# Kernel optimization log

Hardware: AMD Instinct MI355X
Metric: run time of the kernel (lower is better)

## Reference

```python
import jax, jax.numpy as jnp
import numpy as np

NUM_HEADS = 16
D_MODEL = 1024
HEAD_DIM = D_MODEL // NUM_HEADS
SCALE = float(np.sqrt(HEAD_DIM))  # NOTE: original multiplies q by sqrt(head_dim)
EPS = 1e-5


def layernorm(x, g, b):
    # LayerNorm over last dim (head_dim), learnable affine
    mu = jnp.mean(x, axis=-1, keepdims=True)
    var = jnp.mean(jnp.square(x - mu), axis=-1, keepdims=True)
    return (x - mu) * jax.lax.rsqrt(var + EPS) * g + b


def setup_inputs() -> dict:
    key = jax.random.key(0)
    ks = jax.random.split(key, 8)
    B, Nq, Nc = 2, 2048, 2048
    s = 0.02
    return {
        "x_query": jax.random.normal(ks[0], (B, Nq, D_MODEL), jnp.float32),
        "x_context": jax.random.normal(ks[1], (B, Nc, D_MODEL), jnp.float32),
        "Wq": jax.random.normal(ks[2], (D_MODEL, D_MODEL), jnp.float32) * s,
        "Wkv": jax.random.normal(ks[3], (D_MODEL, 2 * D_MODEL), jnp.float32) * s,
        "Wp": jax.random.normal(ks[4], (D_MODEL, D_MODEL), jnp.float32) * s,
        "bp": jnp.zeros((D_MODEL,), jnp.float32),
        "ln_g": jnp.ones((HEAD_DIM,), jnp.float32),
        "ln_b": jnp.zeros((HEAD_DIM,), jnp.float32),
    }


def reference(x_query, x_context, Wq, Wkv, Wp, bp, ln_g, ln_b):
    B, Nq, _ = x_query.shape
    Nc = x_context.shape[1]
    H, D = NUM_HEADS, HEAD_DIM
    # projections
    q = (x_query @ Wq).reshape(B, Nq, H, D).transpose(0, 2, 1, 3)  # b h n d
    kv = (x_context @ Wkv).reshape(B, Nc, 2, H, D)
    k = kv[:, :, 0].transpose(0, 2, 1, 3)  # b h n d
    v = kv[:, :, 1].transpose(0, 2, 1, 3)
    # QK-LayerNorm (shared params)
    q = layernorm(q, ln_g, ln_b)
    k = layernorm(k, ln_g, ln_b)
    # NOTE: faithful to source — q is MULTIPLIED by sqrt(head_dim)
    q = q * SCALE
    attn = jnp.einsum("bhqd,bhkd->bhqk", q, k)
    attn = jax.nn.softmax(attn, axis=-1)
    out = jnp.einsum("bhqk,bhkd->bhqd", attn, v)
    out = out.transpose(0, 2, 1, 3).reshape(B, Nq, H * D)
    return out @ Wp + bp
```

## Files before the change

kernel.cpp:

```cpp
#include <hip/hip_runtime.h>
#include <stdint.h>

#define NUM_HEADS 16
#define HEAD_DIM 64
#define D_MODEL 1024
#define SEQ 2048
#define BATCH 2

typedef unsigned short u16;
typedef __bf16 bf16x8 __attribute__((ext_vector_type(8)));
typedef _Float16 f16x8 __attribute__((ext_vector_type(8)));
typedef float f32x4 __attribute__((ext_vector_type(4)));

__device__ __forceinline__ u16 f2bf(float f) {
    union { float f; uint32_t u; } v; v.f = f;
    uint32_t u = v.u;
    u += 0x7FFFu + ((u >> 16) & 1u);
    return (u16)(u >> 16);
}
__device__ __forceinline__ float bf2f(u16 h) {
    union { uint32_t u; float f; } v; v.u = (uint32_t)h << 16; return v.f;
}
__device__ __forceinline__ u16 f2h(float f) {
    _Float16 h = (_Float16)f;
    return __builtin_bit_cast(u16, h);
}

__device__ __forceinline__ bf16x8 ld8(const u16* p) {
    return *reinterpret_cast<const bf16x8*>(p);
}
__device__ __forceinline__ f16x8 ld8h(const u16* p) {
    return *reinterpret_cast<const f16x8*>(p);
}

__device__ __forceinline__ void gl_lds16(const void* g, void* l) {
    __builtin_amdgcn_global_load_lds(
        (const __attribute__((address_space(1))) void*)g,
        (__attribute__((address_space(3))) void*)l,
        16, 0, 0);
}

template <int CTRL>
__device__ __forceinline__ float dpp_mov(float x) {
    return __builtin_bit_cast(float,
        __builtin_amdgcn_update_dpp(0, __builtin_bit_cast(int, x), CTRL, 0xf, 0xf, true));
}
__device__ __forceinline__ float rowsum16(float x) {
    x += dpp_mov<0x121>(x);
    x += dpp_mov<0x122>(x);
    x += dpp_mov<0x124>(x);
    x += dpp_mov<0x128>(x);
    return x;
}

__global__ __launch_bounds__(256) void k_cast_f16(const float* __restrict__ a,
                                                  const float* __restrict__ b,
                                                  u16* __restrict__ a16,
                                                  u16* __restrict__ b16, int n4each) {
    int i = blockIdx.x * 256 + threadIdx.x;
    const float* src; u16* dst; int j;
    if (i < n4each) { src = a; dst = a16; j = i; }
    else            { src = b; dst = b16; j = i - n4each; }
    float4 v = reinterpret_cast<const float4*>(src)[j];
    ushort4 o;
    o.x = f2h(v.x); o.y = f2h(v.y); o.z = f2h(v.z); o.w = f2h(v.w);
    reinterpret_cast<ushort4*>(dst)[j] = o;
}

__global__ __launch_bounds__(256) void k_transpose_bf16(const float* __restrict__ W,
                                                        u16* __restrict__ WT,
                                                        int K, int N) {
    __shared__ float tile[32][33];
    int bn = blockIdx.x * 32;
    int bk = blockIdx.y * 32;
    int tx = threadIdx.x & 31;
    int ty = threadIdx.x >> 5;
#pragma unroll
    for (int i = 0; i < 32; i += 8)
        tile[ty + i][tx] = W[(size_t)(bk + ty + i) * N + bn + tx];
    __syncthreads();
#pragma unroll
    for (int i = 0; i < 32; i += 8)
        WT[(size_t)(bn + ty + i) * K + bk + tx] = f2bf(tile[tx][ty + i]);
}
__global__ __launch_bounds__(256) void k_transpose_f16(const float* __restrict__ W,
                                                       u16* __restrict__ WT,
                                                       int K, int N) {
    __shared__ float tile[32][33];
    int bn = blockIdx.x * 32;
    int bk = blockIdx.y * 32;
    int tx = threadIdx.x & 31;
    int ty = threadIdx.x >> 5;
#pragma unroll
    for (int i = 0; i < 32; i += 8)
        tile[ty + i][tx] = W[(size_t)(bk + ty + i) * N + bn + tx];
    __syncthreads();
#pragma unroll
    for (int i = 0; i < 32; i += 8)
        WT[(size_t)(bn + ty + i) * K + bk + tx] = f2h(tile[tx][ty + i]);
}

__device__ __forceinline__ void gemm_mainloop(const u16* __restrict__ A,
                                              const u16* __restrict__ Bt,
                                              u16* As, u16* Bs,
                                              int tileM, int tileN, int K,
                                              f32x4 acc[4][4]) {
    const int tid = threadIdx.x;
    const int lane = tid & 63;
    const int wv = tid >> 6;
    const int wm = wv >> 1, wn = wv & 1;
    const int quad = lane >> 4, l15 = lane & 15;

    const int c0 = tid, c1 = tid + 256;
    const u16* Ap0 = A + (size_t)(tileM + (c0 >> 2)) * K + (c0 & 3) * 8;
    const u16* Ap1 = A + (size_t)(tileM + (c1 >> 2)) * K + (c1 & 3) * 8;
    const u16* Bp0 = Bt + (size_t)(tileN + (c0 >> 2)) * K + (c0 & 3) * 8;
    const u16* Bp1 = Bt + (size_t)(tileN + (c1 >> 2)) * K + (c1 & 3) * 8;

    for (int k0 = 0; k0 < K; k0 += 32) {
        __syncthreads();
        gl_lds16(Ap0 + k0, &As[c0 * 8]);
        gl_lds16(Ap1 + k0, &As[c1 * 8]);
        gl_lds16(Bp0 + k0, &Bs[c0 * 8]);
        gl_lds16(Bp1 + k0, &Bs[c1 * 8]);
        __syncthreads();
        bf16x8 af[4], bfr[4];
#pragma unroll
        for (int mi = 0; mi < 4; ++mi)
            af[mi] = ld8(&As[(wm * 64 + mi * 16 + l15) * 32 + quad * 8]);
#pragma unroll
        for (int ni = 0; ni < 4; ++ni)
            bfr[ni] = ld8(&Bs[(wn * 64 + ni * 16 + l15) * 32 + quad * 8]);
#pragma unroll
        for (int mi = 0; mi < 4; ++mi)
#pragma unroll
            for (int ni = 0; ni < 4; ++ni)
                acc[mi][ni] = __builtin_amdgcn_mfma_f32_16x16x32_bf16(
                    af[mi], bfr[ni], acc[mi][ni], 0, 0, 0);
    }
}

__device__ __forceinline__ void gemm_mainloop_f16(const u16* __restrict__ A,
                                                  const u16* __restrict__ Bt,
                                                  u16* As, u16* Bs,
                                                  int tileM, int tileN, int K,
                                                  f32x4 acc[4][4]) {
    const int tid = threadIdx.x;
    const int lane = tid & 63;
    const int wv = tid >> 6;
    const int wm = wv >> 1, wn = wv & 1;
    const int quad = lane >> 4, l15 = lane & 15;

    const int c0 = tid, c1 = tid + 256;
    const u16* Ap0 = A + (size_t)(tileM + (c0 >> 2)) * K + (c0 & 3) * 8;
    const u16* Ap1 = A + (size_t)(tileM + (c1 >> 2)) * K + (c1 & 3) * 8;
    const u16* Bp0 = Bt + (size_t)(tileN + (c0 >> 2)) * K + (c0 & 3) * 8;
    const u16* Bp1 = Bt + (size_t)(tileN + (c1 >> 2)) * K + (c1 & 3) * 8;

    for (int k0 = 0; k0 < K; k0 += 32) {
        __syncthreads();
        gl_lds16(Ap0 + k0, &As[c0 * 8]);
        gl_lds16(Ap1 + k0, &As[c1 * 8]);
        gl_lds16(Bp0 + k0, &Bs[c0 * 8]);
        gl_lds16(Bp1 + k0, &Bs[c1 * 8]);
        __syncthreads();
        f16x8 af[4], bfr[4];
#pragma unroll
        for (int mi = 0; mi < 4; ++mi)
            af[mi] = ld8h(&As[(wm * 64 + mi * 16 + l15) * 32 + quad * 8]);
#pragma unroll
        for (int ni = 0; ni < 4; ++ni)
            bfr[ni] = ld8h(&Bs[(wn * 64 + ni * 16 + l15) * 32 + quad * 8]);
#pragma unroll
        for (int mi = 0; mi < 4; ++mi)
#pragma unroll
            for (int ni = 0; ni < 4; ++ni)
                acc[mi][ni] = __builtin_amdgcn_mfma_f32_16x16x32_f16(
                    af[mi], bfr[ni], acc[mi][ni], 0, 0, 0);
    }
}

#define ACC_INIT()                                                   \
    f32x4 acc[4][4];                                                 \
    _Pragma("unroll") for (int i = 0; i < 4; ++i)                    \
        _Pragma("unroll") for (int j = 0; j < 4; ++j)                \
            acc[i][j] = (f32x4){0.f, 0.f, 0.f, 0.f};

__global__ __launch_bounds__(256, 2) void k_proj_f16(const u16* __restrict__ xq16,
                                                     const u16* __restrict__ xc16,
                                                     const u16* __restrict__ WqT16,
                                                     const u16* __restrict__ WkvT16,
                                                     const float* __restrict__ lng,
                                                     const float* __restrict__ lnb,
                                                     u16* __restrict__ Qh_h,
                                                     u16* __restrict__ Qh_l,
                                                     u16* __restrict__ Kh_h,
                                                     u16* __restrict__ Kh_l,
                                                     u16* __restrict__ VT) {
    __shared__ __align__(16) u16 As[128 * 32];
    __shared__ __align__(16) u16 Bs[128 * 32];
    const int bx = blockIdx.x;
    const int tileM = blockIdx.y * 128;
    const int tid = threadIdx.x;
    const int lane = tid & 63;
    const int wv = tid >> 6;
    const int wm = wv >> 1, wn = wv & 1;
    const int quad = lane >> 4, l15 = lane & 15;
    ACC_INIT();

    if (bx < 16) {
        const bool isQ = bx < 8;
        const int tileN = (bx & 7) * 128;
        const u16* Axx = isQ ? xq16 : xc16;
        const u16* Bt  = isQ ? WqT16 : WkvT16;
        u16* Dh = isQ ? Qh_h : Kh_h;
        u16* Dl = isQ ? Qh_l : Kh_l;
        const float scl = isQ ? 8.0f : 1.0f;

        gemm_mainloop_f16(Axx, Bt, As, Bs, tileM, tileN, D_MODEL, acc);

        float gv[4], bv[4];
#pragma unroll
        for (int ni = 0; ni < 4; ++ni) { gv[ni] = lng[ni * 16 + l15]; bv[ni] = lnb[ni * 16 + l15]; }

#pragma unroll
        for (int mi = 0; mi < 4; ++mi) {
#pragma unroll
            for (int r = 0; r < 4; ++r) {
                float sum = 0.f, sq = 0.f;
#pragma unroll
                for (int ni = 0; ni < 4; ++ni) { float x = acc[mi][ni][r]; sum += x; sq += x * x; }
                sum = rowsum16(sum);
                sq  = rowsum16(sq);
                float mu = sum * (1.f / 64.f);
                float var = sq * (1.f / 64.f) - mu * mu;
                float rs = rsqrtf(var + 1e-5f);
                int m = tileM + wm * 64 + mi * 16 + quad * 4 + r;
                int bb = m >> 11, n = m & (SEQ - 1);
#pragma unroll
                for (int ni = 0; ni < 4; ++ni) {
                    int colg = tileN + wn * 64 + ni * 16 + l15;
                    int h = colg >> 6;
                    float y = ((acc[mi][ni][r] - mu) * rs * gv[ni] + bv[ni]) * scl;
                    size_t idx = (((size_t)bb * NUM_HEADS + h) * SEQ + n) * HEAD_DIM + (colg & 63);
                    u16 yh = f2bf(y);
                    Dh[idx] = yh;
                    Dl[idx] = f2bf(y - bf2f(yh));
                }
            }
        }
    } else {
        const int tileN = D_MODEL + (bx - 16) * 128;
        gemm_mainloop_f16(xc16, WkvT16, As, Bs, tileM, tileN, D_MODEL, acc);
#pragma unroll
        for (int mi = 0; mi < 4; ++mi) {
            int m0 = tileM + wm * 64 + mi * 16 + quad * 4;
            int bb = m0 >> 11, n0 = m0 & (SEQ - 1);
#pragma unroll
            for (int ni = 0; ni < 4; ++ni) {
                int colg = tileN + wn * 64 + ni * 16 + l15 - D_MODEL;
                int h = colg >> 6, d = colg & 63;
                ushort4 o;
                o.x = f2bf(acc[mi][ni][0]);
                o.y = f2bf(acc[mi][ni][1]);
                o.z = f2bf(acc[mi][ni][2]);
                o.w = f2bf(acc[mi][ni][3]);
                *reinterpret_cast<ushort4*>(
                    &VT[(((size_t)bb * NUM_HEADS + h) * HEAD_DIM + d) * SEQ + n0]) = o;
            }
        }
    }
}

__global__ __launch_bounds__(256, 2) void k_gemm_out(const u16* __restrict__ A,
                                                     const u16* __restrict__ Bt,
                                                     const float* __restrict__ bp,
                                                     float* __restrict__ out) {
    __shared__ __align__(16) u16 As[128 * 32];
    __shared__ __align__(16) u16 Bs[128 * 32];
    const int tileM = blockIdx.y * 128, tileN = blockIdx.x * 128;
    const int tid = threadIdx.x;
    const int lane = tid & 63;
    const int wv = tid >> 6;
    const int wm = wv >> 1, wn = wv & 1;
    const int quad = lane >> 4, l15 = lane & 15;
    ACC_INIT();
    gemm_mainloop(A, Bt, As, Bs, tileM, tileN, D_MODEL, acc);

    float bpv[4];
#pragma unroll
    for (int ni = 0; ni < 4; ++ni) bpv[ni] = bp[tileN + wn * 64 + ni * 16 + l15];
#pragma unroll
    for (int mi = 0; mi < 4; ++mi) {
#pragma unroll
        for (int r = 0; r < 4; ++r) {
            int m = tileM + wm * 64 + mi * 16 + quad * 4 + r;
#pragma unroll
            for (int ni = 0; ni < 4; ++ni) {
                int colg = tileN + wn * 64 + ni * 16 + l15;
                out[(size_t)m * D_MODEL + colg] = acc[mi][ni][r] + bpv[ni];
            }
        }
    }
}

__global__ __launch_bounds__(256) void k_attn(const u16* __restrict__ Qh_h,
                                              const u16* __restrict__ Qh_l,
                                              const u16* __restrict__ Kh_h,
                                              const u16* __restrict__ Kh_l,
                                              const u16* __restrict__ VT,
                                              u16* __restrict__ AO) {
    __shared__ __align__(16) u16 Ksh[64 * 64];
    __shared__ __align__(16) u16 Ksl[64 * 64];
    __shared__ __align__(16) u16 Vs[64 * 64];
    __shared__ __align__(16) u16 Ps[64 * 72];

    const int tid = threadIdx.x;
    const int lane = tid & 63;
    const int wv = tid >> 6;
    const int quad = lane >> 4, l15 = lane & 15;
    const int id = blockIdx.x;
    const int bh = (id & 7) | (((id >> 8) & 3) << 3);
    const int qt = (id >> 3) & 31;

    const size_t bh_off = (size_t)bh * SEQ * HEAD_DIM;
    const u16* Qbh_h = Qh_h + bh_off;
    const u16* Qbh_l = Qh_l + bh_off;
    const u16* Vbh = VT + (size_t)bh * HEAD_DIM * SEQ;

    bf16x8 qfh[2], qfl[2];
#pragma unroll
    for (int kt = 0; kt < 2; ++kt) {
        size_t off = (size_t)(qt * 64 + wv * 16 + l15) * HEAD_DIM + kt * 32 + quad * 8;
        qfh[kt] = ld8(Qbh_h + off);
        qfl[kt] = ld8(Qbh_l + off);
    }

    const int rr = lane >> 3;
    const int ss = lane & 7;
    const int cc = ss ^ rr;
    const int row0 = wv * 16 + rr;
    const u16* kh0 = Kh_h + bh_off + (size_t)row0 * HEAD_DIM + cc * 8;
    const u16* kl0 = Kh_l + bh_off + (size_t)row0 * HEAD_DIM + cc * 8;
    const u16* v0  = Vbh + (size_t)row0 * SEQ + cc * 8;
    u16* ldsK0h = &Ksh[(wv * 16) * 64];
    u16* ldsK1h = &Ksh[(wv * 16 + 8) * 64];
    u16* ldsK0l = &Ksl[(wv * 16) * 64];
    u16* ldsK1l = &Ksl[(wv * 16 + 8) * 64];
    u16* ldsV0  = &Vs[(wv * 16) * 64];
    u16* ldsV1  = &Vs[(wv * 16 + 8) * 64];

    f32x4 acc_o[4];
    float m_i = -3.0e38f, l_i = 0.f;
#pragma unroll
    for (int ni = 0; ni < 4; ++ni) acc_o[ni] = (f32x4){0.f, 0.f, 0.f, 0.f};

    for (int j = 0; j < SEQ / 64; ++j) {
        __syncthreads();
        gl_lds16(kh0 + (size_t)j * 64 * HEAD_DIM,                ldsK0h);
        gl_lds16(kh0 + (size_t)j * 64 * HEAD_DIM + 8 * HEAD_DIM, ldsK1h);
        gl_lds16(kl0 + (size_t)j * 64 * HEAD_DIM,                ldsK0l);
        gl_lds16(kl0 + (size_t)j * 64 * HEAD_DIM + 8 * HEAD_DIM, ldsK1l);
        gl_lds16(v0 + j * 64,                                    ldsV0);
        gl_lds16(v0 + j * 64 + (size_t)8 * SEQ,                  ldsV1);
        __syncthreads();

        f32x4 acc_s[4];
#pragma unroll
        for (int ni = 0; ni < 4; ++ni) acc_s[ni] = (f32x4){0.f, 0.f, 0.f, 0.f};
#pragma unroll
        for (int kt = 0; kt < 2; ++kt) {
            bf16x8 kfh[4], kfl[4];
#pragma unroll
            for (int ni = 0; ni < 4; ++ni) {
                int slot = (kt * 4 + quad) ^ (l15 & 7);
                kfh[ni] = ld8(&Ksh[(ni * 16 + l15) * 64 + slot * 8]);
                kfl[ni] = ld8(&Ksl[(ni * 16 + l15) * 64 + slot * 8]);
            }
#pragma unroll
            for (int ni = 0; ni < 4; ++ni) {
                acc_s[ni] = __builtin_amdgcn_mfma_f32_16x16x32_bf16(
                    kfh[ni], qfh[kt], acc_s[ni], 0, 0, 0);
                acc_s[ni] = __builtin_amdgcn_mfma_f32_16x16x32_bf16(
                    kfh[ni], qfl[kt], acc_s[ni], 0, 0, 0);
                acc_s[ni] = __builtin_amdgcn_mfma_f32_16x16x32_bf16(
                    kfl[ni], qfh[kt], acc_s[ni], 0, 0, 0);
            }
        }

        float mx = acc_s[0][0];
#pragma unroll
        for (int ni = 0; ni < 4; ++ni)
#pragma unroll
            for (int r = 0; r < 4; ++r) mx = fmaxf(mx, acc_s[ni][r]);
        mx = fmaxf(mx, __shfl_xor(mx, 16, 64));
        mx = fmaxf(mx, __shfl_xor(mx, 32, 64));
        float mnew = fmaxf(m_i, mx);
        float alpha = __expf(m_i - mnew);
        float sum = 0.f;
        const int psBase = (wv * 16 + l15) * 72;
#pragma unroll
        for (int ni = 0; ni < 4; ++ni) {
            ushort4 pq;
            u16* pp = (u16*)&pq;
#pragma unroll
            for (int r = 0; r < 4; ++r) {
                float p = __expf(acc_s[ni][r] - mnew);
                uint32_t ub = __builtin_bit_cast(uint32_t, p) & 0xffff0000u;
                sum += __builtin_bit_cast(float, ub);
                pp[r] = (u16)(ub >> 16);
            }
            *reinterpret_cast<ushort4*>(&Ps[psBase + ni * 16 + quad * 4]) = pq;
        }
        sum += __shfl_xor(sum, 16, 64);
        sum += __shfl_xor(sum, 32, 64);
        m_i = mnew;
        l_i = l_i * alpha + sum;
#pragma unroll
        for (int ni = 0; ni < 4; ++ni) acc_o[ni] *= alpha;

#pragma unroll
        for (int kt = 0; kt < 2; ++kt) {
            bf16x8 pf = ld8(&Ps[psBase + kt * 32 + quad * 8]);
            bf16x8 vf[4];
#pragma unroll
            for (int ni = 0; ni < 4; ++ni) {
                int slot = (kt * 4 + quad) ^ (l15 & 7);
                vf[ni] = ld8(&Vs[(ni * 16 + l15) * 64 + slot * 8]);
            }
#pragma unroll
            for (int ni = 0; ni < 4; ++ni)
                acc_o[ni] = __builtin_amdgcn_mfma_f32_16x16x32_bf16(
                    vf[ni], pf, acc_o[ni], 0, 0, 0);
        }
    }

    const float inv = 1.0f / l_i;
    const int psBase = (wv * 16 + l15) * 72;
#pragma unroll
    for (int ni = 0; ni < 4; ++ni) {
        ushort4 oq;
        u16* op = (u16*)&oq;
#pragma unroll
        for (int r = 0; r < 4; ++r) op[r] = f2bf(acc_o[ni][r] * inv);
        *reinterpret_cast<ushort4*>(&Ps[psBase + ni * 16 + quad * 4]) = oq;
    }
    const int b = bh >> 4, h = bh & 15;
    const int qrow = qt * 64 + wv * 16 + l15;
    bf16x8 o0 = ld8(&Ps[psBase + quad * 16]);
    bf16x8 o1 = ld8(&Ps[psBase + quad * 16 + 8]);
    size_t outb = ((size_t)(b * SEQ + qrow)) * D_MODEL + h * 64 + quad * 16;
    *reinterpret_cast<uint4*>(&AO[outb])     = __builtin_bit_cast(uint4, o0);
    *reinterpret_cast<uint4*>(&AO[outb + 8]) = __builtin_bit_cast(uint4, o1);
}

extern "C" void kernel_launch(void* const* d_in, const int* in_sizes, int n_in,
                              void* d_out, int out_size, void* d_ws, size_t ws_size,
                              hipStream_t stream) {
    const float* xq  = (const float*)d_in[0];
    const float* xc  = (const float*)d_in[1];
    const float* Wq  = (const float*)d_in[2];
    const float* Wkv = (const float*)d_in[3];
    const float* Wp  = (const float*)d_in[4];
    const float* bp  = (const float*)d_in[5];
    const float* lng = (const float*)d_in[6];
    const float* lnb = (const float*)d_in[7];
    float* out = (float*)d_out;

    char* ws = (char*)d_ws;
    const size_t MB = 1 << 20;
    u16* xq16   = (u16*)(ws + 0 * MB);
    u16* xc16   = (u16*)(ws + 8 * MB);
    u16* WqT16  = (u16*)(ws + 16 * MB);
    u16* WkvT16 = (u16*)(ws + 18 * MB);
    u16* WpT    = (u16*)(ws + 22 * MB);
    u16* Qh_h   = (u16*)(ws + 24 * MB);
    u16* Qh_l   = (u16*)(ws + 32 * MB);
    u16* Kh_h   = (u16*)(ws + 40 * MB);
    u16* Kh_l   = (u16*)(ws + 48 * MB);
    u16* VT     = (u16*)(ws + 56 * MB);
    u16* AO     = xq16;

    k_cast_f16<<<8192, 256, 0, stream>>>(xq, xc, xq16, xc16, 1048576);
    k_transpose_f16<<<dim3(32, 32), 256, 0, stream>>>(Wq, WqT16, 1024, 1024);
    k_transpose_f16<<<dim3(64, 32), 256, 0, stream>>>(Wkv, WkvT16, 1024, 2048);
    k_transpose_bf16<<<dim3(32, 32), 256, 0, stream>>>(Wp, WpT, 1024, 1024);

    k_proj_f16<<<dim3(24, 32), 256, 0, stream>>>(xq16, xc16, WqT16, WkvT16,
                                                 lng, lnb, Qh_h, Qh_l, Kh_h, Kh_l, VT);
    k_attn<<<1024, 256, 0, stream>>>(Qh_h, Qh_l, Kh_h, Kh_l, VT, AO);
    k_gemm_out<<<dim3(8, 32), 256, 0, stream>>>(AO, WpT, bp, out);
}
```

Baseline: 277.6 us.

## Fuse prep kernels, double-buffer attention K/V loads, switch P/V/out to fp16

```diff
diff --git a/kernel.cpp b/kernel.cpp
--- a/kernel.cpp
+++ b/kernel.cpp
@@ -24,6 +24,9 @@
 __device__ __forceinline__ u16 f2h(float f) {
     _Float16 h = (_Float16)f;
     return __builtin_bit_cast(u16, h);
+}
+__device__ __forceinline__ uint32_t pkrtz(float a, float b) {
+    return __builtin_bit_cast(uint32_t, __builtin_amdgcn_cvt_pkrtz(a, b));
 }
 
 __device__ __forceinline__ bf16x8 ld8(const u16* p) {
@@ -53,91 +56,45 @@
     return x;
 }
 
-__global__ __launch_bounds__(256) void k_cast_f16(const float* __restrict__ a,
-                                                  const float* __restrict__ b,
-                                                  u16* __restrict__ a16,
-                                                  u16* __restrict__ b16, int n4each) {
-    int i = blockIdx.x * 256 + threadIdx.x;
-    const float* src; u16* dst; int j;
-    if (i < n4each) { src = a; dst = a16; j = i; }
-    else            { src = b; dst = b16; j = i - n4each; }
-    float4 v = reinterpret_cast<const float4*>(src)[j];
-    ushort4 o;
-    o.x = f2h(v.x); o.y = f2h(v.y); o.z = f2h(v.z); o.w = f2h(v.w);
-    reinterpret_cast<ushort4*>(dst)[j] = o;
-}
-
-__global__ __launch_bounds__(256) void k_transpose_bf16(const float* __restrict__ W,
-                                                        u16* __restrict__ WT,
-                                                        int K, int N) {
+__global__ __launch_bounds__(256) void k_prep(const float* __restrict__ xq,
+                                              const float* __restrict__ xc,
+                                              const float* __restrict__ Wq,
+                                              const float* __restrict__ Wkv,
+                                              const float* __restrict__ Wp,
+                                              u16* __restrict__ xq16,
+                                              u16* __restrict__ xc16,
+                                              u16* __restrict__ WqT16,
+                                              u16* __restrict__ WkvT16,
+                                              u16* __restrict__ WpT16) {
     __shared__ float tile[32][33];
-    int bn = blockIdx.x * 32;
-    int bk = blockIdx.y * 32;
-    int tx = threadIdx.x & 31;
-    int ty = threadIdx.x >> 5;
+    const int t = blockIdx.x;
+    if (t < 8192) {
+        int i = t * 256 + threadIdx.x;
+        const float* src; u16* dst; int j;
+        if (i < 1048576) { src = xq; dst = xq16; j = i; }
+        else             { src = xc; dst = xc16; j = i - 1048576; }
+        float4 v = reinterpret_cast<const float4*>(src)[j];
+        ushort4 o;
+        o.x = f2h(v.x); o.y = f2h(v.y); o.z = f2h(v.z); o.w = f2h(v.w);
+        reinterpret_cast<ushort4*>(dst)[j] = o;
+        return;
+    }
+    const float* W; u16* WT; int N, bi;
+    if (t < 9216)       { W = Wq;  WT = WqT16;  N = 1024; bi = t - 8192; }
+    else if (t < 11264) { W = Wkv; WT = WkvT16; N = 2048; bi = t - 9216; }
+    else                { W = Wp;  WT = WpT16;  N = 1024; bi = t - 11264; }
+    const int K = 1024;
+    const int nb = N / 32;
+    const int bn = (bi % nb) * 32, bk = (bi / nb) * 32;
+    const int tx = threadIdx.x & 31;
+    const int ty = threadIdx.x >> 5;
 #pragma unroll
     for (int i = 0; i < 32; i += 8)
         tile[ty + i][tx] = W[(size_t)(bk + ty + i) * N + bn + tx];
     __syncthreads();
 #pragma unroll
     for (int i = 0; i < 32; i += 8)
-        WT[(size_t)(bn + ty + i) * K + bk + tx] = f2bf(tile[tx][ty + i]);
-}
-__global__ __launch_bounds__(256) void k_transpose_f16(const float* __restrict__ W,
-                                                       u16* __restrict__ WT,
-                                                       int K, int N) {
-    __shared__ float tile[32][33];
-    int bn = blockIdx.x * 32;
-    int bk = blockIdx.y * 32;
-    int tx = threadIdx.x & 31;
-    int ty = threadIdx.x >> 5;
-#pragma unroll
-    for (int i = 0; i < 32; i += 8)
-        tile[ty + i][tx] = W[(size_t)(bk + ty + i) * N + bn + tx];
-    __syncthreads();
-#pragma unroll
-    for (int i = 0; i < 32; i += 8)
         WT[(size_t)(bn + ty + i) * K + bk + tx] = f2h(tile[tx][ty + i]);
-}
-
-__device__ __forceinline__ void gemm_mainloop(const u16* __restrict__ A,
-                                              const u16* __restrict__ Bt,
-                                              u16* As, u16* Bs,
-                                              int tileM, int tileN, int K,
-                                              f32x4 acc[4][4]) {
-    const int tid = threadIdx.x;
-    const int lane = tid & 63;
-    const int wv = tid >> 6;
-    const int wm = wv >> 1, wn = wv & 1;
-    const int quad = lane >> 4, l15 = lane & 15;
-
-    const int c0 = tid, c1 = tid + 256;
-    const u16* Ap0 = A + (size_t)(tileM + (c0 >> 2)) * K + (c0 & 3) * 8;
-    const u16* Ap1 = A + (size_t)(tileM + (c1 >> 2)) * K + (c1 & 3) * 8;
-    const u16* Bp0 = Bt + (size_t)(tileN + (c0 >> 2)) * K + (c0 & 3) * 8;
-    const u16* Bp1 = Bt + (size_t)(tileN + (c1 >> 2)) * K + (c1 & 3) * 8;
-
-    for (int k0 = 0; k0 < K; k0 += 32) {
-        __syncthreads();
-        gl_lds16(Ap0 + k0, &As[c0 * 8]);
-        gl_lds16(Ap1 + k0, &As[c1 * 8]);
-        gl_lds16(Bp0 + k0, &Bs[c0 * 8]);
-        gl_lds16(Bp1 + k0, &Bs[c1 * 8]);
-        __syncthreads();
-        bf16x8 af[4], bfr[4];
-#pragma unroll
-        for (int mi = 0; mi < 4; ++mi)
-            af[mi] = ld8(&As[(wm * 64 + mi * 16 + l15) * 32 + quad * 8]);
-#pragma unroll
-        for (int ni = 0; ni < 4; ++ni)
-            bfr[ni] = ld8(&Bs[(wn * 64 + ni * 16 + l15) * 32 + quad * 8]);
-#pragma unroll
-        for (int mi = 0; mi < 4; ++mi)
-#pragma unroll
-            for (int ni = 0; ni < 4; ++ni)
-                acc[mi][ni] = __builtin_amdgcn_mfma_f32_16x16x32_bf16(
-                    af[mi], bfr[ni], acc[mi][ni], 0, 0, 0);
-    }
 }
 
 __device__ __forceinline__ void gemm_mainloop_f16(const u16* __restrict__ A,
@@ -261,10 +218,10 @@
                 int colg = tileN + wn * 64 + ni * 16 + l15 - D_MODEL;
                 int h = colg >> 6, d = colg & 63;
                 ushort4 o;
-                o.x = f2bf(acc[mi][ni][0]);
-                o.y = f2bf(acc[mi][ni][1]);
-                o.z = f2bf(acc[mi][ni][2]);
-                o.w = f2bf(acc[mi][ni][3]);
+                o.x = f2h(acc[mi][ni][0]);
+                o.y = f2h(acc[mi][ni][1]);
+                o.z = f2h(acc[mi][ni][2]);
+                o.w = f2h(acc[mi][ni][3]);
                 *reinterpret_cast<ushort4*>(
                     &VT[(((size_t)bb * NUM_HEADS + h) * HEAD_DIM + d) * SEQ + n0]) = o;
             }
@@ -285,7 +242,7 @@
     const int wm = wv >> 1, wn = wv & 1;
     const int quad = lane >> 4, l15 = lane & 15;
     ACC_INIT();
-    gemm_mainloop(A, Bt, As, Bs, tileM, tileN, D_MODEL, acc);
+    gemm_mainloop_f16(A, Bt, As, Bs, tileM, tileN, D_MODEL, acc);
 
     float bpv[4];
 #pragma unroll
@@ -310,9 +267,9 @@
                                               const u16* __restrict__ Kh_l,
                                               const u16* __restrict__ VT,
                                               u16* __restrict__ AO) {
-    __shared__ __align__(16) u16 Ksh[64 * 64];
-    __shared__ __align__(16) u16 Ksl[64 * 64];
-    __shared__ __align__(16) u16 Vs[64 * 64];
+    __shared__ __align__(16) u16 Ksh[2 * 64 * 64];
+    __shared__ __align__(16) u16 Ksl[2 * 64 * 64];
+    __shared__ __align__(16) u16 Vs[2 * 64 * 64];
     __shared__ __align__(16) u16 Ps[64 * 72];
 
     const int tid = threadIdx.x;
@@ -343,27 +300,36 @@
     const u16* kh0 = Kh_h + bh_off + (size_t)row0 * HEAD_DIM + cc * 8;
     const u16* kl0 = Kh_l + bh_off + (size_t)row0 * HEAD_DIM + cc * 8;
     const u16* v0  = Vbh + (size_t)row0 * SEQ + cc * 8;
-    u16* ldsK0h = &Ksh[(wv * 16) * 64];
-    u16* ldsK1h = &Ksh[(wv * 16 + 8) * 64];
-    u16* ldsK0l = &Ksl[(wv * 16) * 64];
-    u16* ldsK1l = &Ksl[(wv * 16 + 8) * 64];
-    u16* ldsV0  = &Vs[(wv * 16) * 64];
-    u16* ldsV1  = &Vs[(wv * 16 + 8) * 64];
+    const int ldsW = (wv * 16) * 64;
 
     f32x4 acc_o[4];
     float m_i = -3.0e38f, l_i = 0.f;
 #pragma unroll
     for (int ni = 0; ni < 4; ++ni) acc_o[ni] = (f32x4){0.f, 0.f, 0.f, 0.f};
 
+    {
+        gl_lds16(kh0,                 &Ksh[ldsW]);
+        gl_lds16(kh0 + 8 * HEAD_DIM,  &Ksh[ldsW + 8 * 64]);
+        gl_lds16(kl0,                 &Ksl[ldsW]);
+        gl_lds16(kl0 + 8 * HEAD_DIM,  &Ksl[ldsW + 8 * 64]);
+        gl_lds16(v0,                  &Vs[ldsW]);
+        gl_lds16(v0 + 8 * SEQ,        &Vs[ldsW + 8 * 64]);
+    }
+
     for (int j = 0; j < SEQ / 64; ++j) {
         __syncthreads();
-        gl_lds16(kh0 + (size_t)j * 64 * HEAD_DIM,                ldsK0h);
-        gl_lds16(kh0 + (size_t)j * 64 * HEAD_DIM + 8 * HEAD_DIM, ldsK1h);
-        gl_lds16(kl0 + (size_t)j * 64 * HEAD_DIM,                ldsK0l);
-        gl_lds16(kl0 + (size_t)j * 64 * HEAD_DIM + 8 * HEAD_DIM, ldsK1l);
-        gl_lds16(v0 + j * 64,                                    ldsV0);
-        gl_lds16(v0 + j * 64 + (size_t)8 * SEQ,                  ldsV1);
-        __syncthreads();
+        if (j + 1 < SEQ / 64) {
+            const int nb = (j + 1) & 1;
+            const size_t ko = (size_t)(j + 1) * 64 * HEAD_DIM;
+            const int vo = (j + 1) * 64;
+            gl_lds16(kh0 + ko,                 &Ksh[nb * 4096 + ldsW]);
+            gl_lds16(kh0 + ko + 8 * HEAD_DIM,  &Ksh[nb * 4096 + ldsW + 8 * 64]);
+            gl_lds16(kl0 + ko,                 &Ksl[nb * 4096 + ldsW]);
+            gl_lds16(kl0 + ko + 8 * HEAD_DIM,  &Ksl[nb * 4096 + ldsW + 8 * 64]);
+            gl_lds16(v0 + vo,                  &Vs[nb * 4096 + ldsW]);
+            gl_lds16(v0 + vo + 8 * SEQ,        &Vs[nb * 4096 + ldsW + 8 * 64]);
+        }
+        const int bb = (j & 1) * 4096;
 
         f32x4 acc_s[4];
 #pragma unroll
@@ -374,8 +340,8 @@
 #pragma unroll
             for (int ni = 0; ni < 4; ++ni) {
                 int slot = (kt * 4 + quad) ^ (l15 & 7);
-                kfh[ni] = ld8(&Ksh[(ni * 16 + l15) * 64 + slot * 8]);
-                kfl[ni] = ld8(&Ksl[(ni * 16 + l15) * 64 + slot * 8]);
+                kfh[ni] = ld8(&Ksh[bb + (ni * 16 + l15) * 64 + slot * 8]);
+                kfl[ni] = ld8(&Ksl[bb + (ni * 16 + l15) * 64 + slot * 8]);
             }
 #pragma unroll
             for (int ni = 0; ni < 4; ++ni) {
@@ -401,16 +367,15 @@
         const int psBase = (wv * 16 + l15) * 72;
 #pragma unroll
         for (int ni = 0; ni < 4; ++ni) {
-            ushort4 pq;
-            u16* pp = (u16*)&pq;
-#pragma unroll
-            for (int r = 0; r < 4; ++r) {
-                float p = __expf(acc_s[ni][r] - mnew);
-                uint32_t ub = __builtin_bit_cast(uint32_t, p) & 0xffff0000u;
-                sum += __builtin_bit_cast(float, ub);
-                pp[r] = (u16)(ub >> 16);
-            }
-            *reinterpret_cast<ushort4*>(&Ps[psBase + ni * 16 + quad * 4]) = pq;
+            float p0 = __expf(acc_s[ni][0] - mnew);
+            float p1 = __expf(acc_s[ni][1] - mnew);
+            float p2 = __expf(acc_s[ni][2] - mnew);
+            float p3 = __expf(acc_s[ni][3] - mnew);
+            sum += (p0 + p1) + (p2 + p3);
+            uint2 u;
+            u.x = pkrtz(p0, p1);
+            u.y = pkrtz(p2, p3);
+            *reinterpret_cast<uint2*>(&Ps[psBase + ni * 16 + quad * 4]) = u;
         }
         sum += __shfl_xor(sum, 16, 64);
         sum += __shfl_xor(sum, 32, 64);
@@ -421,16 +386,16 @@
 
 #pragma unroll
         for (int kt = 0; kt < 2; ++kt) {
-            bf16x8 pf = ld8(&Ps[psBase + kt * 32 + quad * 8]);
-            bf16x8 vf[4];
+            f16x8 pf = ld8h(&Ps[psBase + kt * 32 + quad * 8]);
+            f16x8 vf[4];
 #pragma unroll
             for (int ni = 0; ni < 4; ++ni) {
                 int slot = (kt * 4 + quad) ^ (l15 & 7);
-                vf[ni] = ld8(&Vs[(ni * 16 + l15) * 64 + slot * 8]);
+                vf[ni] = ld8h(&Vs[bb + (ni * 16 + l15) * 64 + slot * 8]);
             }
 #pragma unroll
             for (int ni = 0; ni < 4; ++ni)
-                acc_o[ni] = __builtin_amdgcn_mfma_f32_16x16x32_bf16(
+                acc_o[ni] = __builtin_amdgcn_mfma_f32_16x16x32_f16(
                     vf[ni], pf, acc_o[ni], 0, 0, 0);
         }
     }
@@ -439,19 +404,18 @@
     const int psBase = (wv * 16 + l15) * 72;
 #pragma unroll
     for (int ni = 0; ni < 4; ++ni) {
-        ushort4 oq;
-        u16* op = (u16*)&oq;
-#pragma unroll
-        for (int r = 0; r < 4; ++r) op[r] = f2bf(acc_o[ni][r] * inv);
-        *reinterpret_cast<ushort4*>(&Ps[psBase + ni * 16 + quad * 4]) = oq;
+        uint2 u;
+        u.x = pkrtz(acc_o[ni][0] * inv, acc_o[ni][1] * inv);
+        u.y = pkrtz(acc_o[ni][2] * inv, acc_o[ni][3] * inv);
+        *reinterpret_cast<uint2*>(&Ps[psBase + ni * 16 + quad * 4]) = u;
     }
     const int b = bh >> 4, h = bh & 15;
     const int qrow = qt * 64 + wv * 16 + l15;
-    bf16x8 o0 = ld8(&Ps[psBase + quad * 16]);
-    bf16x8 o1 = ld8(&Ps[psBase + quad * 16 + 8]);
+    uint4 o0 = *reinterpret_cast<const uint4*>(&Ps[psBase + quad * 16]);
+    uint4 o1 = *reinterpret_cast<const uint4*>(&Ps[psBase + quad * 16 + 8]);
     size_t outb = ((size_t)(b * SEQ + qrow)) * D_MODEL + h * 64 + quad * 16;
-    *reinterpret_cast<uint4*>(&AO[outb])     = __builtin_bit_cast(uint4, o0);
-    *reinterpret_cast<uint4*>(&AO[outb + 8]) = __builtin_bit_cast(uint4, o1);
+    *reinterpret_cast<uint4*>(&AO[outb])     = o0;
+    *reinterpret_cast<uint4*>(&AO[outb + 8]) = o1;
 }
 
 extern "C" void kernel_launch(void* const* d_in, const int* in_sizes, int n_in,
@@ -473,7 +437,7 @@
     u16* xc16   = (u16*)(ws + 8 * MB);
     u16* WqT16  = (u16*)(ws + 16 * MB);
     u16* WkvT16 = (u16*)(ws + 18 * MB);
-    u16* WpT    = (u16*)(ws + 22 * MB);
+    u16* WpT16  = (u16*)(ws + 22 * MB);
     u16* Qh_h   = (u16*)(ws + 24 * MB);
     u16* Qh_l   = (u16*)(ws + 32 * MB);
     u16* Kh_h   = (u16*)(ws + 40 * MB);
@@ -481,13 +445,10 @@
     u16* VT     = (u16*)(ws + 56 * MB);
     u16* AO     = xq16;
 
-    k_cast_f16<<<8192, 256, 0, stream>>>(xq, xc, xq16, xc16, 1048576);
-    k_transpose_f16<<<dim3(32, 32), 256, 0, stream>>>(Wq, WqT16, 1024, 1024);
-    k_transpose_f16<<<dim3(64, 32), 256, 0, stream>>>(Wkv, WkvT16, 1024, 2048);
-    k_transpose_bf16<<<dim3(32, 32), 256, 0, stream>>>(Wp, WpT, 1024, 1024);
-
+    k_prep<<<12288, 256, 0, stream>>>(xq, xc, Wq, Wkv, Wp,
+                                      xq16, xc16, WqT16, WkvT16, WpT16);
     k_proj_f16<<<dim3(24, 32), 256, 0, stream>>>(xq16, xc16, WqT16, WkvT16,
                                                  lng, lnb, Qh_h, Qh_l, Kh_h, Kh_l, VT);
     k_attn<<<1024, 256, 0, stream>>>(Qh_h, Qh_l, Kh_h, Kh_l, VT, AO);
-    k_gemm_out<<<dim3(8, 32), 256, 0, stream>>>(AO, WpT, bp, out);
-}
+    k_gemm_out<<<dim3(8, 32), 256, 0, stream>>>(AO, WpT16, bp, out);
+}
```

New measurement: 274.7 us. About the same (-1.0%).
